# Performance work log

Hardware: AMD Instinct MI355X
Metric: run time of the kernel (lower is better)

Reference implementation:

```python
import jax, jax.numpy as jnp
import numpy as np

N_NODES = 100000
N_EDGES = 1600000
D_FEAT = 128
N_CLASSES = 16


def setup_inputs() -> dict:
    key = jax.random.key(0)
    ks = jax.random.split(key, 7)
    return {
        "x": jax.random.normal(ks[0], (N_NODES, D_FEAT), dtype=jnp.float32),
        "edge_row": jax.random.randint(ks[1], (N_EDGES,), 0, N_NODES),
        "edge_col": jax.random.randint(ks[2], (N_EDGES,), 0, N_NODES),
        "edge_val": jax.random.uniform(ks[3], (N_EDGES,), dtype=jnp.float32),
        "w1": jax.random.normal(ks[4], (D_FEAT, D_FEAT), dtype=jnp.float32) * 0.05,
        "w2": jax.random.normal(ks[5], (D_FEAT, D_FEAT), dtype=jnp.float32) * 0.05,
        "classifier": jax.random.normal(ks[6], (D_FEAT, N_CLASSES), dtype=jnp.float32) * 0.05,
    }


def reference(x, edge_row, edge_col, edge_val, w1, w2, classifier):
    n = x.shape[0]

    def spmm(h):
        # Adj.dot(h): gather source node features, scale by edge weight, scatter-add to rows
        msgs = edge_val[:, None] * h[edge_col]          # [E, D]
        return jax.ops.segment_sum(msgs, edge_row, num_segments=n)  # [N, D]

    h = x
    for w in (w1, w2):
        h = jax.nn.relu(spmm(h) @ w)
    logits = h @ classifier                              # [N, C]
    # x[x>0]=1; x[x<=0]=0  -> hard binary threshold
    return jnp.where(logits > 0, jnp.float32(1.0), jnp.float32(0.0))
```

## Files before the change

### kernel.cpp

```cpp
#include <hip/hip_runtime.h>
#include <climits>

#define D 128
#define TR 32
#define TS 132

typedef float f32x4 __attribute__((ext_vector_type(4)));
typedef float f32x2 __attribute__((ext_vector_type(2)));
typedef int   i32x2 __attribute__((ext_vector_type(2)));

__global__ __launch_bounds__(256) void hist_rank_kernel(const int* __restrict__ erow,
                                                        int* __restrict__ deg,
                                                        int* __restrict__ rank, int nE) {
    int e = blockIdx.x * 256 + threadIdx.x;
    if (e < nE) rank[e] = atomicAdd(&deg[erow[e]], 1);
}

__global__ __launch_bounds__(256) void scan1_kernel(const int* __restrict__ deg,
                                                    int* __restrict__ rowptr,
                                                    int* __restrict__ blocksums, int n) {
    __shared__ int sd[256];
    const int t = threadIdx.x;
    const int idx = blockIdx.x * 1024 + t * 4;
    int4 v = make_int4(0, 0, 0, 0);
    if (idx + 3 < n) v = *(const int4*)&deg[idx];
    else {
        if (idx + 0 < n) v.x = deg[idx + 0];
        if (idx + 1 < n) v.y = deg[idx + 1];
        if (idx + 2 < n) v.z = deg[idx + 2];
        if (idx + 3 < n) v.w = deg[idx + 3];
    }
    const int s = v.x + v.y + v.z + v.w;
    sd[t] = s;
    __syncthreads();
    for (int off = 1; off < 256; off <<= 1) {
        int tv = (t >= off) ? sd[t - off] : 0;
        __syncthreads();
        sd[t] += tv;
        __syncthreads();
    }
    const int excl = sd[t] - s;
    int a = excl + v.x, b = a + v.y, c = b + v.z, d = c + v.w;
    if (idx + 0 < n) rowptr[idx + 1] = a;
    if (idx + 1 < n) rowptr[idx + 2] = b;
    if (idx + 2 < n) rowptr[idx + 3] = c;
    if (idx + 3 < n) rowptr[idx + 4] = d;
    if (t == 255) blocksums[blockIdx.x] = sd[255];
}

__global__ __launch_bounds__(256) void scan2_kernel(int* __restrict__ blocksums, int nb) {
    __shared__ int sd[256];
    const int t = threadIdx.x;
    const int v = (t < nb) ? blocksums[t] : 0;
    sd[t] = v;
    __syncthreads();
    for (int off = 1; off < 256; off <<= 1) {
        int tv = (t >= off) ? sd[t - off] : 0;
        __syncthreads();
        sd[t] += tv;
        __syncthreads();
    }
    if (t < nb) blocksums[t] = sd[t] - v;
}

__global__ __launch_bounds__(256) void scan3_kernel(int* __restrict__ rowptr,
                                                    const int* __restrict__ blocksums, int n) {
    int i = blockIdx.x * 256 + threadIdx.x;
    if (i < n) rowptr[i + 1] += blocksums[i >> 10];
    if (i == 0) rowptr[0] = 0;
}

__global__ __launch_bounds__(256) void place_kernel(const int* __restrict__ erow,
                                                    const int* __restrict__ rank,
                                                    const int* __restrict__ ecol,
                                                    const float* __restrict__ ev,
                                                    const int* __restrict__ rowptr,
                                                    i32x2* __restrict__ cv, int nE) {
    int e = blockIdx.x * 256 + threadIdx.x;
    if (e >= nE) return;
    int pos = rowptr[erow[e]] + rank[e];
    i32x2 rec;
    rec.x = ecol[e];
    rec.y = __float_as_int(ev[e]);
    cv[pos] = rec;
}

__global__ __launch_bounds__(256) void sortrow_wave_kernel(const int* __restrict__ rowptr,
                                                           i32x2* __restrict__ cv, int n) {
    int row = blockIdx.x * 4 + (threadIdx.x >> 6);
    if (row >= n) return;
    const int lane = threadIdx.x & 63;
    const int s = rowptr[row], e = rowptr[row + 1];
    const int deg = e - s;
    if (deg <= 1) return;
    if (deg <= 64) {
        unsigned long long key = ~0ull;
        i32x2 rec;
        rec.x = 0; rec.y = 0;
        if (lane < deg) {
            rec = cv[s + lane];
            key = ((unsigned long long)(unsigned)rec.x << 32) | (unsigned)rec.y;
        }
        int rank = 0;
        for (int i = 0; i < deg; ++i) {
            unsigned long long ki = __shfl(key, i);
            rank += (ki < key || (ki == key && i < lane)) ? 1 : 0;
        }
        if (lane < deg) cv[s + rank] = rec;
    } else if (lane == 0) {
        for (int i = s + 1; i < e; ++i) {
            i32x2 r_ = cv[i];
            unsigned long long k_ = ((unsigned long long)(unsigned)r_.x << 32) | (unsigned)r_.y;
            int j = i - 1;
            while (j >= s) {
                i32x2 rj = cv[j];
                unsigned long long kj = ((unsigned long long)(unsigned)rj.x << 32) | (unsigned)rj.y;
                if (kj <= k_) break;
                cv[j + 1] = rj;
                --j;
            }
            cv[j + 1] = r_;
        }
    }
}

template <bool CLASSIFY>
__global__ __launch_bounds__(256, 4) void fused_layer_kernel(
        const float* __restrict__ h, const int* __restrict__ rowptr,
        const i32x2* __restrict__ cv, const float* __restrict__ W,
        const float* __restrict__ Cls, float* __restrict__ O, int n) {
    __shared__ float tile[TR * TS];
    __shared__ float cls_s[CLASSIFY ? D * 16 : 1];

    if (CLASSIFY) {
        for (int i = threadIdx.x * 8; i < D * 16; i += 256 * 8) {
            *(f32x4*)&cls_s[i]     = *(const f32x4*)&Cls[i];
            *(f32x4*)&cls_s[i + 4] = *(const f32x4*)&Cls[i + 4];
        }
    }

    const int row0 = blockIdx.x * TR;

    {
        const int rp = threadIdx.x >> 5;
        const int l = threadIdx.x & 31;
        const f32x4* hl = (const f32x4*)h + l;
        for (int i = 0; i < 4; ++i) {
            const int rl = i * 8 + rp;
            const int r = row0 + rl;
            f32x4 acc = (f32x4)(0.f);
            if (r < n) {
                const int s = rowptr[r], e = rowptr[r + 1];
                int k = s;
                for (; k + 8 <= e; k += 8) {
                    i32x2 p[8];
#pragma unroll
                    for (int u = 0; u < 8; ++u) p[u] = cv[k + u];
                    f32x4 hv[8];
#pragma unroll
                    for (int u = 0; u < 8; ++u) hv[u] = hl[(size_t)p[u].x * 32];
#pragma unroll
                    for (int u = 0; u < 8; ++u) acc += __int_as_float(p[u].y) * hv[u];
                }
                for (; k < e; ++k) {
                    i32x2 p = cv[k];
                    acc += __int_as_float(p.y) * hl[(size_t)p.x * 32];
                }
            }
            *(f32x4*)&tile[rl * TS + l * 4] = acc;
        }
    }
    __syncthreads();

    const int cg = threadIdx.x & 15;
    const int rq = threadIdx.x >> 4;
    const int c0 = cg * 8;

    float acc[2][8];
#pragma unroll
    for (int r = 0; r < 2; ++r)
#pragma unroll
        for (int c = 0; c < 8; ++c) acc[r][c] = 0.f;

    for (int k = 0; k < D; k += 4) {
        f32x4 a[2];
#pragma unroll
        for (int r = 0; r < 2; ++r) a[r] = *(const f32x4*)&tile[(rq * 2 + r) * TS + k];
#pragma unroll
        for (int kk = 0; kk < 4; ++kk) {
            const float* wrow = &W[(k + kk) * D + c0];
            f32x4 w0 = *(const f32x4*)&wrow[0];
            f32x4 w1 = *(const f32x4*)&wrow[4];
#pragma unroll
            for (int r = 0; r < 2; ++r) {
                float av = a[r][kk];
                acc[r][0] += av * w0.x; acc[r][1] += av * w0.y;
                acc[r][2] += av * w0.z; acc[r][3] += av * w0.w;
                acc[r][4] += av * w1.x; acc[r][5] += av * w1.y;
                acc[r][6] += av * w1.z; acc[r][7] += av * w1.w;
            }
        }
    }

    if (!CLASSIFY) {
#pragma unroll
        for (int r = 0; r < 2; ++r) {
            int row = row0 + rq * 2 + r;
            if (row >= n) continue;
            f32x4 v0, v1;
            v0.x = fmaxf(acc[r][0], 0.f); v0.y = fmaxf(acc[r][1], 0.f);
            v0.z = fmaxf(acc[r][2], 0.f); v0.w = fmaxf(acc[r][3], 0.f);
            v1.x = fmaxf(acc[r][4], 0.f); v1.y = fmaxf(acc[r][5], 0.f);
            v1.z = fmaxf(acc[r][6], 0.f); v1.w = fmaxf(acc[r][7], 0.f);
            *(f32x4*)&O[(size_t)row * D + c0]     = v0;
            *(f32x4*)&O[(size_t)row * D + c0 + 4] = v1;
        }
    } else {
        __syncthreads();
#pragma unroll
        for (int r = 0; r < 2; ++r) {
            f32x4 v0, v1;
            v0.x = fmaxf(acc[r][0], 0.f); v0.y = fmaxf(acc[r][1], 0.f);
            v0.z = fmaxf(acc[r][2], 0.f); v0.w = fmaxf(acc[r][3], 0.f);
            v1.x = fmaxf(acc[r][4], 0.f); v1.y = fmaxf(acc[r][5], 0.f);
            v1.z = fmaxf(acc[r][6], 0.f); v1.w = fmaxf(acc[r][7], 0.f);
            *(f32x4*)&tile[(rq * 2 + r) * TS + c0]     = v0;
            *(f32x4*)&tile[(rq * 2 + r) * TS + c0 + 4] = v1;
        }
        __syncthreads();
        const int rl = threadIdx.x >> 3;
        const int q = threadIdx.x & 7;
        float lg0 = 0.f, lg1 = 0.f;
        for (int k = 0; k < D; ++k) {
            float hv = tile[rl * TS + k];
            lg0 += hv * cls_s[k * 16 + q * 2];
            lg1 += hv * cls_s[k * 16 + q * 2 + 1];
        }
        int row = row0 + rl;
        if (row < n) {
            f32x2 o;
            o.x = lg0 > 0.f ? 1.f : 0.f;
            o.y = lg1 > 0.f ? 1.f : 0.f;
            *(f32x2*)&O[(size_t)row * 16 + q * 2] = o;
        }
    }
}

extern "C" void kernel_launch(void* const* d_in, const int* in_sizes, int n_in,
                              void* d_out, int out_size, void* d_ws, size_t ws_size,
                              hipStream_t stream) {
    const float* x    = (const float*)d_in[0];
    const int*   erow = (const int*)d_in[1];
    const int*   ecol = (const int*)d_in[2];
    const float* ev   = (const float*)d_in[3];
    const float* w1   = (const float*)d_in[4];
    const float* w2   = (const float*)d_in[5];
    const float* cls  = (const float*)d_in[6];

    const int n  = in_sizes[0] / D;
    const int nE = in_sizes[1];

    char*  ws     = (char*)d_ws;
    float* h      = (float*)ws;                 ws += (size_t)n * D * 4;
    int*   deg    = (int*)ws;                   ws += (size_t)n * 4;
    int*   rowptr = (int*)ws;                   ws += (size_t)(n + 1) * 4;
    int*   rank   = (int*)ws;                   ws += (size_t)nE * 4;
    i32x2* cv     = (i32x2*)ws;                 ws += (size_t)nE * 8;
    int*   bsums  = (int*)ws;                   ws += 256 * 4;

    const int nb = (n + 1023) / 1024;

    dim3 blk(256);
    dim3 egrid((nE + 255) / 256);
    dim3 ngrid((n + 255) / 256);
    dim3 wgrid((n + 3) / 4);
    dim3 fgrid((n + TR - 1) / TR);

    (void)hipMemsetAsync(deg, 0, (size_t)n * 4, stream);
    hist_rank_kernel<<<egrid, blk, 0, stream>>>(erow, deg, rank, nE);
    scan1_kernel<<<nb, blk, 0, stream>>>(deg, rowptr, bsums, n);
    scan2_kernel<<<1, blk, 0, stream>>>(bsums, nb);
    scan3_kernel<<<ngrid, blk, 0, stream>>>(rowptr, bsums, n);
    place_kernel<<<egrid, blk, 0, stream>>>(erow, rank, ecol, ev, rowptr, cv, nE);
    sortrow_wave_kernel<<<wgrid, blk, 0, stream>>>(rowptr, cv, n);

    fused_layer_kernel<false><<<fgrid, blk, 0, stream>>>(x, rowptr, cv, w1, nullptr, h, n);

    fused_layer_kernel<true><<<fgrid, blk, 0, stream>>>(h, rowptr, cv, w2, cls,
                                                        (float*)d_out, n);
}
```

Before: 523.9 us.

## Replace shared-memory tile with per-wave register shuffles in fused SpMM-GEMM

Each 64-lane wave now owns 8 rows. Two half-waves each aggregate neighbor features into registers, and the dense W multiply and classifier are done with cross-lane shuffles instead of an LDS tile and __syncthreads. This removes the shared-memory staging and block barriers, and drops the occupancy hint from launch bounds. In exchange it issues many shuffles per FMA and re-reads W and the classifier from global/L1 per wave rather than sharing them across the block.

```diff
diff --git a/kernel.cpp b/kernel.cpp
--- a/kernel.cpp
+++ b/kernel.cpp
@@ -2,11 +2,8 @@
 #include <climits>
 
 #define D 128
-#define TR 32
-#define TS 132
 
 typedef float f32x4 __attribute__((ext_vector_type(4)));
-typedef float f32x2 __attribute__((ext_vector_type(2)));
 typedef int   i32x2 __attribute__((ext_vector_type(2)));
 
 __global__ __launch_bounds__(256) void hist_rank_kernel(const int* __restrict__ erow,
@@ -125,123 +122,104 @@
 }
 
 template <bool CLASSIFY>
-__global__ __launch_bounds__(256, 4) void fused_layer_kernel(
+__global__ __launch_bounds__(256) void spmm_gemm_kernel(
         const float* __restrict__ h, const int* __restrict__ rowptr,
         const i32x2* __restrict__ cv, const float* __restrict__ W,
         const float* __restrict__ Cls, float* __restrict__ O, int n) {
-    __shared__ float tile[TR * TS];
-    __shared__ float cls_s[CLASSIFY ? D * 16 : 1];
-
-    if (CLASSIFY) {
-        for (int i = threadIdx.x * 8; i < D * 16; i += 256 * 8) {
-            *(f32x4*)&cls_s[i]     = *(const f32x4*)&Cls[i];
-            *(f32x4*)&cls_s[i + 4] = *(const f32x4*)&Cls[i + 4];
-        }
-    }
-
-    const int row0 = blockIdx.x * TR;
-
-    {
-        const int rp = threadIdx.x >> 5;
-        const int l = threadIdx.x & 31;
-        const f32x4* hl = (const f32x4*)h + l;
+    const int wid = (blockIdx.x * 256 + threadIdx.x) >> 6;
+    const int lane = threadIdx.x & 63;
+    const int half = lane >> 5;
+    const int l = lane & 31;
+    const int row0 = wid * 8;
+    if (row0 >= n) return;
+
+    const f32x4* hl = (const f32x4*)h + l;
+    f32x4 rowdata[4];
+#pragma unroll
+    for (int i = 0; i < 4; ++i) {
+        const int r = row0 + 2 * i + half;
+        f32x4 acc = (f32x4)(0.f);
+        if (r < n) {
+            const int s = rowptr[r], e = rowptr[r + 1];
+            int k = s;
+            for (; k + 8 <= e; k += 8) {
+                i32x2 p[8];
+#pragma unroll
+                for (int u = 0; u < 8; ++u) p[u] = cv[k + u];
+                f32x4 hv[8];
+#pragma unroll
+                for (int u = 0; u < 8; ++u) hv[u] = hl[(size_t)p[u].x * 32];
+#pragma unroll
+                for (int u = 0; u < 8; ++u) acc += __int_as_float(p[u].y) * hv[u];
+            }
+            for (; k < e; ++k) {
+                i32x2 p = cv[k];
+                acc += __int_as_float(p.y) * hl[(size_t)p.x * 32];
+            }
+        }
+        rowdata[i] = acc;
+    }
+
+    const int c0 = l * 4;
+    const int sbase = half << 5;
+    f32x4 oacc[4];
+#pragma unroll
+    for (int i = 0; i < 4; ++i) oacc[i] = (f32x4)(0.f);
+
+    for (int k4 = 0; k4 < D / 4; ++k4) {
+        const int srcl = sbase + k4;
+#pragma unroll
+        for (int kk = 0; kk < 4; ++kk) {
+            const f32x4 w = *(const f32x4*)&W[(k4 * 4 + kk) * D + c0];
+#pragma unroll
+            for (int i = 0; i < 4; ++i) {
+                float hk = __shfl(rowdata[i][kk], srcl);
+                oacc[i] += hk * w;
+            }
+        }
+    }
+
+    if (!CLASSIFY) {
+#pragma unroll
         for (int i = 0; i < 4; ++i) {
-            const int rl = i * 8 + rp;
-            const int r = row0 + rl;
-            f32x4 acc = (f32x4)(0.f);
+            const int r = row0 + 2 * i + half;
             if (r < n) {
-                const int s = rowptr[r], e = rowptr[r + 1];
-                int k = s;
-                for (; k + 8 <= e; k += 8) {
-                    i32x2 p[8];
-#pragma unroll
-                    for (int u = 0; u < 8; ++u) p[u] = cv[k + u];
-                    f32x4 hv[8];
-#pragma unroll
-                    for (int u = 0; u < 8; ++u) hv[u] = hl[(size_t)p[u].x * 32];
-#pragma unroll
-                    for (int u = 0; u < 8; ++u) acc += __int_as_float(p[u].y) * hv[u];
+                f32x4 v;
+                v.x = fmaxf(oacc[i].x, 0.f); v.y = fmaxf(oacc[i].y, 0.f);
+                v.z = fmaxf(oacc[i].z, 0.f); v.w = fmaxf(oacc[i].w, 0.f);
+                *(f32x4*)&O[(size_t)r * D + c0] = v;
+            }
+        }
+    } else {
+#pragma unroll
+        for (int i = 0; i < 4; ++i) {
+            oacc[i].x = fmaxf(oacc[i].x, 0.f); oacc[i].y = fmaxf(oacc[i].y, 0.f);
+            oacc[i].z = fmaxf(oacc[i].z, 0.f); oacc[i].w = fmaxf(oacc[i].w, 0.f);
+        }
+        const int j = l & 15;
+        const int kh = l >> 4;
+        float lg[4] = {0.f, 0.f, 0.f, 0.f};
+        for (int m4 = 0; m4 < 16; ++m4) {
+            const int srcl = sbase + kh * 16 + m4;
+#pragma unroll
+            for (int kk = 0; kk < 4; ++kk) {
+                const int k = kh * 64 + m4 * 4 + kk;
+                const float c = Cls[k * 16 + j];
+#pragma unroll
+                for (int i = 0; i < 4; ++i) {
+                    float hk = __shfl(oacc[i][kk], srcl);
+                    lg[i] += hk * c;
                 }
-                for (; k < e; ++k) {
-                    i32x2 p = cv[k];
-                    acc += __int_as_float(p.y) * hl[(size_t)p.x * 32];
-                }
-            }
-            *(f32x4*)&tile[rl * TS + l * 4] = acc;
-        }
-    }
-    __syncthreads();
-
-    const int cg = threadIdx.x & 15;
-    const int rq = threadIdx.x >> 4;
-    const int c0 = cg * 8;
-
-    float acc[2][8];
-#pragma unroll
-    for (int r = 0; r < 2; ++r)
-#pragma unroll
-        for (int c = 0; c < 8; ++c) acc[r][c] = 0.f;
-
-    for (int k = 0; k < D; k += 4) {
-        f32x4 a[2];
-#pragma unroll
-        for (int r = 0; r < 2; ++r) a[r] = *(const f32x4*)&tile[(rq * 2 + r) * TS + k];
-#pragma unroll
-        for (int kk = 0; kk < 4; ++kk) {
-            const float* wrow = &W[(k + kk) * D + c0];
-            f32x4 w0 = *(const f32x4*)&wrow[0];
-            f32x4 w1 = *(const f32x4*)&wrow[4];
-#pragma unroll
-            for (int r = 0; r < 2; ++r) {
-                float av = a[r][kk];
-                acc[r][0] += av * w0.x; acc[r][1] += av * w0.y;
-                acc[r][2] += av * w0.z; acc[r][3] += av * w0.w;
-                acc[r][4] += av * w1.x; acc[r][5] += av * w1.y;
-                acc[r][6] += av * w1.z; acc[r][7] += av * w1.w;
-            }
-        }
-    }
-
-    if (!CLASSIFY) {
-#pragma unroll
-        for (int r = 0; r < 2; ++r) {
-            int row = row0 + rq * 2 + r;
-            if (row >= n) continue;
-            f32x4 v0, v1;
-            v0.x = fmaxf(acc[r][0], 0.f); v0.y = fmaxf(acc[r][1], 0.f);
-            v0.z = fmaxf(acc[r][2], 0.f); v0.w = fmaxf(acc[r][3], 0.f);
-            v1.x = fmaxf(acc[r][4], 0.f); v1.y = fmaxf(acc[r][5], 0.f);
-            v1.z = fmaxf(acc[r][6], 0.f); v1.w = fmaxf(acc[r][7], 0.f);
-            *(f32x4*)&O[(size_t)row * D + c0]     = v0;
-            *(f32x4*)&O[(size_t)row * D + c0 + 4] = v1;
-        }
-    } else {
-        __syncthreads();
-#pragma unroll
-        for (int r = 0; r < 2; ++r) {
-            f32x4 v0, v1;
-            v0.x = fmaxf(acc[r][0], 0.f); v0.y = fmaxf(acc[r][1], 0.f);
-            v0.z = fmaxf(acc[r][2], 0.f); v0.w = fmaxf(acc[r][3], 0.f);
-            v1.x = fmaxf(acc[r][4], 0.f); v1.y = fmaxf(acc[r][5], 0.f);
-            v1.z = fmaxf(acc[r][6], 0.f); v1.w = fmaxf(acc[r][7], 0.f);
-            *(f32x4*)&tile[(rq * 2 + r) * TS + c0]     = v0;
-            *(f32x4*)&tile[(rq * 2 + r) * TS + c0 + 4] = v1;
-        }
-        __syncthreads();
-        const int rl = threadIdx.x >> 3;
-        const int q = threadIdx.x & 7;
-        float lg0 = 0.f, lg1 = 0.f;
-        for (int k = 0; k < D; ++k) {
-            float hv = tile[rl * TS + k];
-            lg0 += hv * cls_s[k * 16 + q * 2];
-            lg1 += hv * cls_s[k * 16 + q * 2 + 1];
-        }
-        int row = row0 + rl;
-        if (row < n) {
-            f32x2 o;
-            o.x = lg0 > 0.f ? 1.f : 0.f;
-            o.y = lg1 > 0.f ? 1.f : 0.f;
-            *(f32x2*)&O[(size_t)row * 16 + q * 2] = o;
+            }
+        }
+#pragma unroll
+        for (int i = 0; i < 4; ++i) lg[i] += __shfl_xor(lg[i], 16);
+        if (kh == 0) {
+#pragma unroll
+            for (int i = 0; i < 4; ++i) {
+                const int r = row0 + 2 * i + half;
+                if (r < n) O[(size_t)r * 16 + j] = lg[i] > 0.f ? 1.f : 0.f;
+            }
         }
     }
 }
@@ -274,7 +252,7 @@
     dim3 egrid((nE + 255) / 256);
     dim3 ngrid((n + 255) / 256);
     dim3 wgrid((n + 3) / 4);
-    dim3 fgrid((n + TR - 1) / TR);
+    dim3 sgrid((n + 31) / 32);
 
     (void)hipMemsetAsync(deg, 0, (size_t)n * 4, stream);
     hist_rank_kernel<<<egrid, blk, 0, stream>>>(erow, deg, rank, nE);
@@ -284,8 +262,8 @@
     place_kernel<<<egrid, blk, 0, stream>>>(erow, rank, ecol, ev, rowptr, cv, nE);
     sortrow_wave_kernel<<<wgrid, blk, 0, stream>>>(rowptr, cv, n);
 
-    fused_layer_kernel<false><<<fgrid, blk, 0, stream>>>(x, rowptr, cv, w1, nullptr, h, n);
-
-    fused_layer_kernel<true><<<fgrid, blk, 0, stream>>>(h, rowptr, cv, w2, cls,
-                                                        (float*)d_out, n);
-}
+    spmm_gemm_kernel<false><<<sgrid, blk, 0, stream>>>(x, rowptr, cv, w1, nullptr, h, n);
+
+    spmm_gemm_kernel<true><<<sgrid, blk, 0, stream>>>(h, rowptr, cv, w2, cls,
+                                                      (float*)d_out, n);
+}
```

New measurement: 474.4 us. 9.5% less time.
